# Kernel tuning notes

Hardware: AMD Instinct MI355X
Metric: run time of the kernel (lower is better)

## Reference

```python
import jax, jax.numpy as jnp
import numpy as np

R = 8          # num_real
P = 8          # num_complex_conjugate_pairs
L = 4          # num_layers (hidden Linear+ReLU blocks)
H = 256        # hidden_dim
B = 16384      # batch


def _init_params(key, C, out_dim):
    ks = jax.random.split(key, 6)
    s_in = 1.0  # fan_in = 1
    s_h = 1.0 / np.sqrt(H)
    return dict(
        W_in=jax.random.uniform(ks[0], (C, H), jnp.float32, -s_in, s_in),
        b_in=jax.random.uniform(ks[1], (C, H), jnp.float32, -s_in, s_in),
        W_h=jax.random.uniform(ks[2], (L, C, H, H), jnp.float32, -s_h, s_h),
        b_h=jax.random.uniform(ks[3], (L, C, H), jnp.float32, -s_h, s_h),
        W_out=jax.random.uniform(ks[4], (C, out_dim, H), jnp.float32, -s_h, s_h),
        b_out=jax.random.uniform(ks[5], (C, out_dim), jnp.float32, -s_h, s_h),
    )


def setup_inputs() -> dict:
    key = jax.random.key(0)
    kz, kr, kc = jax.random.split(key, 3)
    z = jax.random.normal(kz, (B, R + 2 * P), jnp.float32)
    pr = _init_params(kr, R, 1)   # real-eigenvalue MLPs, out_dim=1
    pc = _init_params(kc, P, 2)   # complex-pair MLPs, out_dim=2
    return {
        "z": z,
        "Wr_in": pr["W_in"], "br_in": pr["b_in"],
        "Wr_h": pr["W_h"], "br_h": pr["b_h"],
        "Wr_out": pr["W_out"], "br_out": pr["b_out"],
        "Wc_in": pc["W_in"], "bc_in": pc["b_in"],
        "Wc_h": pc["W_h"], "bc_h": pc["b_h"],
        "Wc_out": pc["W_out"], "bc_out": pc["b_out"],
    }


def _grouped_mlp(x, W_in, b_in, W_h, b_h, W_out, b_out):
    # x: [B, C] scalar input per channel; all C tiny MLPs run as grouped GEMMs.
    h = jax.nn.relu(x[..., None] * W_in + b_in)            # [B, C, H]
    for l in range(W_h.shape[0]):
        h = jax.nn.relu(jnp.einsum('bci,coi->bco', h, W_h[l]) + b_h[l])
    return jnp.einsum('bci,coi->bco', h, W_out) + b_out     # [B, C, out]


def reference(z, Wr_in, br_in, Wr_h, br_h, Wr_out, br_out,
              Wc_in, bc_in, Wc_h, bc_h, Wc_out, bc_out):
    # real channels: z[..., i] -> Linear chains -> real_lambda [B, R]
    real_lambda = _grouped_mlp(z[..., :R], Wr_in, br_in, Wr_h, br_h,
                               Wr_out, br_out)[..., 0]
    # complex pairs: magnitude z_r^2 + z_i^2 per pair -> (mu, omega)
    z_mag = z[..., R::2] ** 2 + z[..., R + 1::2] ** 2        # [B, P]
    mu_omega = _grouped_mlp(z_mag, Wc_in, bc_in, Wc_h, bc_h,
                            Wc_out, bc_out)                  # [B, P, 2]
    mu = mu_omega[..., 0]
    omega = mu_omega[..., 1]
    return real_lambda, mu, omega
```

## Files before the change

### kernel.cpp

```cpp
#include <hip/hip_runtime.h>

#define OUT_MU 131072
#define OUT_OM 262144
#define BIAS_OFF 4194304
#define WOUT_OFF 4210688

typedef _Float16 half8 __attribute__((ext_vector_type(8)));
typedef _Float16 half4 __attribute__((ext_vector_type(4)));
typedef float    floatx16 __attribute__((ext_vector_type(16)));

__device__ __forceinline__ void wait_lgkm0() {
    asm volatile("s_waitcnt lgkmcnt(0)" ::: "memory");
}
__device__ __forceinline__ void wait_vm0() {
    asm volatile("s_waitcnt vmcnt(0)" ::: "memory");
}
__device__ __forceinline__ void barrier_raw() {
    asm volatile("s_barrier" ::: "memory");
}

#define AS1 __attribute__((address_space(1)))
#define AS3 __attribute__((address_space(3)))

__global__ void prep_w(const float* __restrict__ Wr_h,
                       const float* __restrict__ Wc_h,
                       _Float16* __restrict__ dst) {
    int v = blockIdx.x * 256 + threadIdx.x;
    int lane = v & 63;
    int nt   = (v >> 6) & 1;
    int wv   = (v >> 7) & 3;
    int ks   = (v >> 9) & 15;
    int l    = (v >> 13) & 3;
    int ch   = v >> 15;
    int n  = wv * 64 + nt * 32 + (lane & 31);
    int k0 = ks * 16 + (lane >> 5) * 8;
    const float* src = (ch < 8) ? Wr_h : Wc_h;
    int c = ch & 7;
    const float* p = src + ((size_t)((l * 8 + c) * 256 + n)) * 256 + k0;
    float4 a = *(const float4*)p;
    float4 b = *(const float4*)(p + 4);
    half8 o;
    o[0] = (_Float16)a.x; o[1] = (_Float16)a.y; o[2] = (_Float16)a.z; o[3] = (_Float16)a.w;
    o[4] = (_Float16)b.x; o[5] = (_Float16)b.y; o[6] = (_Float16)b.z; o[7] = (_Float16)b.w;
    *(half8*)(dst + (size_t)v * 8) = o;
}

__global__ void prep_b(const float* __restrict__ br_h,
                       const float* __restrict__ bc_h,
                       _Float16* __restrict__ dst) {
    int t = blockIdx.x * 256 + threadIdx.x;
    int e  = t & 3;
    int q  = (t >> 2) & 3;
    int nt = (t >> 4) & 1;
    int hi = (t >> 5) & 1;
    int wv = (t >> 6) & 3;
    int l  = (t >> 8) & 3;
    int ch = (t >> 10) & 15;
    int n = wv * 64 + nt * 32 + q * 8 + hi * 4 + e;
    const float* src = (ch < 8) ? br_h : bc_h;
    dst[BIAS_OFF + t] = (_Float16)src[(l * 8 + (ch & 7)) * 256 + n];
}

__global__ void prep_wo(const float* __restrict__ Wr_out,
                        const float* __restrict__ Wc_out,
                        _Float16* __restrict__ dst) {
    int t = blockIdx.x * 256 + threadIdx.x;
    int j = t & 255, d = (t >> 8) & 1, ch = t >> 9;
    int c = ch & 7;
    float v;
    if (ch < 8) v = d ? 0.f : Wr_out[c * 256 + j];
    else        v = Wc_out[(c * 2 + d) * 256 + j];
    dst[WOUT_OFF + t] = (_Float16)v;
}

__global__ __launch_bounds__(256, 2)
void mlp_fused(const float* __restrict__ z,
               const float* __restrict__ Wr_in, const float* __restrict__ br_in,
               const float* __restrict__ Wc_in, const float* __restrict__ bc_in,
               const float* __restrict__ br_out, const float* __restrict__ bc_out,
               const _Float16* __restrict__ wst,
               float* __restrict__ out) {
    __shared__ __align__(16) char smem[77824];
    const int tid  = threadIdx.x;
    const int lane = tid & 63;
    const int wv   = tid >> 6;
    const int bid  = blockIdx.x;
    const int ch   = bid & 15;
    const int m0   = (bid >> 4) * 128;
    const bool isC = ch >= 8;
    const int c    = ch & 7;
    const int hi   = lane >> 5;
    const int r32  = lane & 31;
    float* zbuf = (float*)(smem + 65536);

    {
        const float* zs = z + (size_t)m0 * 24 + wv * 768 + lane * 4;
        char* zd = smem + 65536 + wv * 3072;
        __builtin_amdgcn_global_load_lds((const AS1 void*)zs,         (AS3 void*)zd,          16, 0, 0);
        __builtin_amdgcn_global_load_lds((const AS1 void*)(zs + 256), (AS3 void*)(zd + 1024), 16, 0, 0);
        __builtin_amdgcn_global_load_lds((const AS1 void*)(zs + 512), (AS3 void*)(zd + 2048), 16, 0, 0);
    }

    const half8* wl = (const half8*)wst + (size_t)ch * 32768 + wv * 128 + lane;

    half8 wr[2][2];
    #pragma unroll
    for (int nt = 0; nt < 2; ++nt) wr[0][nt] = wl[nt * 64];

    int vb[4];
    #pragma unroll
    for (int mt = 0; mt < 4; ++mt)
        vb[mt] = (mt * 32 + r32) * 512 + ((hi ^ (lane & 7)) << 4);

    const int jg = tid & 31;
    const int rg = tid >> 5;
    const float* Wi = (isC ? Wc_in : Wr_in) + c * 256 + jg * 8;
    const float* bi = (isC ? bc_in : br_in) + c * 256 + jg * 8;
    float4 w0 = *(const float4*)Wi;
    float4 w1 = *(const float4*)(Wi + 4);
    float4 v0 = *(const float4*)bi;
    float4 v1 = *(const float4*)(bi + 4);

    wait_vm0();

    {
        #pragma unroll
        for (int i = 0; i < 16; ++i) {
            int m = rg * 16 + i;
            float x;
            if (!isC) x = zbuf[m * 24 + c];
            else {
                float2 p = *(const float2*)(zbuf + m * 24 + 8 + 2 * c);
                x = p.x * p.x + p.y * p.y;
            }
            half8 o;
            o[0] = (_Float16)fmaxf(fmaf(x, w0.x, v0.x), 0.f);
            o[1] = (_Float16)fmaxf(fmaf(x, w0.y, v0.y), 0.f);
            o[2] = (_Float16)fmaxf(fmaf(x, w0.z, v0.z), 0.f);
            o[3] = (_Float16)fmaxf(fmaf(x, w0.w, v0.w), 0.f);
            o[4] = (_Float16)fmaxf(fmaf(x, w1.x, v1.x), 0.f);
            o[5] = (_Float16)fmaxf(fmaf(x, w1.y, v1.y), 0.f);
            o[6] = (_Float16)fmaxf(fmaf(x, w1.z, v1.z), 0.f);
            o[7] = (_Float16)fmaxf(fmaf(x, w1.w, v1.w), 0.f);
            *(half8*)(smem + m * 512 + ((jg ^ (m & 7)) << 4)) = o;
        }
    }
    wait_lgkm0();
    barrier_raw();

    const half8* bpc = (const half8*)(wst + BIAS_OFF) + ((ch * 4) * 4 + wv) * 8 + hi * 4;

    #pragma unroll 1
    for (int l = 0; l < 4; ++l) {
        const half8* bl = bpc + l * 32;
        half8 bb0 = bl[0], bb1 = bl[1], bb2 = bl[2], bb3 = bl[3];

        floatx16 acc[2][4];
        #pragma unroll
        for (int a = 0; a < 2; ++a)
            #pragma unroll
            for (int b = 0; b < 4; ++b) acc[a][b] = 0.f;

        half8 bfr[2][4];
        #pragma unroll
        for (int mt = 0; mt < 4; ++mt)
            bfr[0][mt] = *(const half8*)(smem + vb[mt]);

        #pragma unroll
        for (int ks = 0; ks < 16; ++ks) {
            {
                const half8* p = wl + (ks + 1) * 512;
                wr[(ks + 1) & 1][0] = p[0];
                wr[(ks + 1) & 1][1] = p[64];
            }
            if (ks < 15) {
                #pragma unroll
                for (int mt = 0; mt < 4; ++mt)
                    bfr[(ks + 1) & 1][mt] =
                        *(const half8*)(smem + (vb[mt] ^ ((ks + 1) << 5)));
            }
            __builtin_amdgcn_s_setprio(1);
            #pragma unroll
            for (int nt = 0; nt < 2; ++nt)
                #pragma unroll
                for (int mt = 0; mt < 4; ++mt)
                    acc[nt][mt] = __builtin_amdgcn_mfma_f32_32x32x16_f16(
                        wr[ks & 1][nt], bfr[ks & 1][mt], acc[nt][mt], 0, 0, 0);
            __builtin_amdgcn_s_setprio(0);
        }
        wl += 8192;

        wait_lgkm0();
        barrier_raw();
        #pragma unroll
        for (int nt = 0; nt < 2; ++nt) {
            #pragma unroll
            for (int q = 0; q < 4; ++q) {
                half8 bv = (nt * 2 + (q >> 1)) == 0 ? bb0 :
                           (nt * 2 + (q >> 1)) == 1 ? bb1 :
                           (nt * 2 + (q >> 1)) == 2 ? bb2 : bb3;
                const int be = (q & 1) * 4;
                float b0 = (float)bv[be + 0];
                float b1 = (float)bv[be + 1];
                float b2 = (float)bv[be + 2];
                float b3 = (float)bv[be + 3];
                const int slot = wv * 8 + nt * 4 + q;
                #pragma unroll
                for (int mt = 0; mt < 4; ++mt) {
                    const int m = mt * 32 + r32;
                    half4 o;
                    o[0] = (_Float16)fmaxf(acc[nt][mt][4 * q + 0] + b0, 0.f);
                    o[1] = (_Float16)fmaxf(acc[nt][mt][4 * q + 1] + b1, 0.f);
                    o[2] = (_Float16)fmaxf(acc[nt][mt][4 * q + 2] + b2, 0.f);
                    o[3] = (_Float16)fmaxf(acc[nt][mt][4 * q + 3] + b3, 0.f);
                    *(half4*)(smem + m * 512 + ((slot ^ (m & 7)) << 4) + hi * 8) = o;
                }
            }
        }
        wait_lgkm0();
        barrier_raw();
    }

    {
        const int q = tid & 1, m = tid >> 1;
        const half8* Wo = (const half8*)(wst + WOUT_OFF) + ch * 64 + q * 16;
        float s0 = 0.f, s1 = 0.f;
        #pragma unroll
        for (int i = 0; i < 16; ++i) {
            int slot = q * 16 + i;
            half8 hv = *(const half8*)(smem + m * 512 + ((slot ^ (m & 7)) << 4));
            half8 wo0 = Wo[i];
            #pragma unroll
            for (int e = 0; e < 8; ++e) s0 = fmaf((float)hv[e], (float)wo0[e], s0);
            if (isC) {
                half8 wo1 = Wo[32 + i];
                #pragma unroll
                for (int e = 0; e < 8; ++e) s1 = fmaf((float)hv[e], (float)wo1[e], s1);
            }
        }
        s0 += __shfl_xor(s0, 1);
        if (isC) s1 += __shfl_xor(s1, 1);
        if (q == 0) {
            const int row = m0 + m;
            if (!isC) {
                out[row * 8 + c] = s0 + br_out[c];
            } else {
                out[OUT_MU + row * 8 + c] = s0 + bc_out[c * 2];
                out[OUT_OM + row * 8 + c] = s1 + bc_out[c * 2 + 1];
            }
        }
    }
}

extern "C" void kernel_launch(void* const* d_in, const int* in_sizes, int n_in,
                              void* d_out, int out_size, void* d_ws, size_t ws_size,
                              hipStream_t stream) {
    const float* z      = (const float*)d_in[0];
    const float* Wr_in  = (const float*)d_in[1];
    const float* br_in  = (const float*)d_in[2];
    const float* Wr_h   = (const float*)d_in[3];
    const float* br_h   = (const float*)d_in[4];
    const float* Wr_out = (const float*)d_in[5];
    const float* br_out = (const float*)d_in[6];
    const float* Wc_in  = (const float*)d_in[7];
    const float* bc_in  = (const float*)d_in[8];
    const float* Wc_h   = (const float*)d_in[9];
    const float* bc_h   = (const float*)d_in[10];
    const float* Wc_out = (const float*)d_in[11];
    const float* bc_out = (const float*)d_in[12];
    _Float16* wst = (_Float16*)d_ws;
    float* out = (float*)d_out;

    prep_w<<<2048, 256, 0, stream>>>(Wr_h, Wc_h, wst);
    prep_b<<<64, 256, 0, stream>>>(br_h, bc_h, wst);
    prep_wo<<<32, 256, 0, stream>>>(Wr_out, Wc_out, wst);
    mlp_fused<<<2048, 256, 0, stream>>>(z, Wr_in, br_in, Wc_in, bc_in,
                                        br_out, bc_out, wst, out);
}
```

Measured before the change: 146.3 us.

## Split each 128-row tile across eight waves with deeper weight prefetch

The fused MLP block grows from 4 to 8 waves. Each wave now computes a 64x64 output tile: waves are split by column group and by row half, so MFMA accumulators per wave drop from 8 to 4. Weight fragments are prefetched two k-steps ahead in a 4-deep register ring, and the output dot product and input layer are spread over more threads. The aim is more latency hiding and higher occupancy, at the cost of each weight fragment being loaded by two waves instead of one. An extra barrier is added after the z load.

```diff
diff --git a/kernel.cpp b/kernel.cpp
--- a/kernel.cpp
+++ b/kernel.cpp
@@ -73,7 +73,7 @@
     dst[WOUT_OFF + t] = (_Float16)v;
 }
 
-__global__ __launch_bounds__(256, 2)
+__global__ __launch_bounds__(512, 4)
 void mlp_fused(const float* __restrict__ z,
                const float* __restrict__ Wr_in, const float* __restrict__ br_in,
                const float* __restrict__ Wc_in, const float* __restrict__ bc_in,
@@ -84,6 +84,8 @@
     const int tid  = threadIdx.x;
     const int lane = tid & 63;
     const int wv   = tid >> 6;
+    const int wr   = wv & 3;
+    const int wc   = wv >> 2;
     const int bid  = blockIdx.x;
     const int ch   = bid & 15;
     const int m0   = (bid >> 4) * 128;
@@ -93,7 +95,7 @@
     const int r32  = lane & 31;
     float* zbuf = (float*)(smem + 65536);
 
-    {
+    if (wv < 4) {
         const float* zs = z + (size_t)m0 * 24 + wv * 768 + lane * 4;
         char* zd = smem + 65536 + wv * 3072;
         __builtin_amdgcn_global_load_lds((const AS1 void*)zs,         (AS3 void*)zd,          16, 0, 0);
@@ -101,16 +103,13 @@
         __builtin_amdgcn_global_load_lds((const AS1 void*)(zs + 512), (AS3 void*)(zd + 2048), 16, 0, 0);
     }
 
-    const half8* wl = (const half8*)wst + (size_t)ch * 32768 + wv * 128 + lane;
-
-    half8 wr[2][2];
-    #pragma unroll
-    for (int nt = 0; nt < 2; ++nt) wr[0][nt] = wl[nt * 64];
-
-    int vb[4];
-    #pragma unroll
-    for (int mt = 0; mt < 4; ++mt)
-        vb[mt] = (mt * 32 + r32) * 512 + ((hi ^ (lane & 7)) << 4);
+    const half8* wl = (const half8*)wst + (size_t)ch * 32768 + wr * 128 + lane;
+
+    half8 wreg[4][2];
+    wreg[0][0] = wl[0];   wreg[0][1] = wl[64];
+    wreg[1][0] = wl[512]; wreg[1][1] = wl[576];
+
+    const int vb = (wc * 64 + r32) * 512 + ((hi ^ (lane & 7)) << 4);
 
     const int jg = tid & 31;
     const int rg = tid >> 5;
@@ -122,11 +121,12 @@
     float4 v1 = *(const float4*)(bi + 4);
 
     wait_vm0();
+    barrier_raw();
 
     {
         #pragma unroll
-        for (int i = 0; i < 16; ++i) {
-            int m = rg * 16 + i;
+        for (int i = 0; i < 8; ++i) {
+            int m = rg * 8 + i;
             float x;
             if (!isC) x = zbuf[m * 24 + c];
             else {
@@ -148,47 +148,47 @@
     wait_lgkm0();
     barrier_raw();
 
-    const half8* bpc = (const half8*)(wst + BIAS_OFF) + ((ch * 4) * 4 + wv) * 8 + hi * 4;
+    const half8* bpc = (const half8*)(wst + BIAS_OFF) + ((ch * 4) * 4 + wr) * 8 + hi * 4;
 
     #pragma unroll 1
     for (int l = 0; l < 4; ++l) {
+        floatx16 acc[2][2];
+        #pragma unroll
+        for (int a = 0; a < 2; ++a)
+            #pragma unroll
+            for (int b = 0; b < 2; ++b) acc[a][b] = 0.f;
+
+        half8 bfr[2][2];
+        bfr[0][0] = *(const half8*)(smem + vb);
+        bfr[0][1] = *(const half8*)(smem + vb + 16384);
+
+        #pragma unroll
+        for (int ks = 0; ks < 16; ++ks) {
+            {
+                const half8* p = wl + (ks + 2) * 512;
+                wreg[(ks + 2) & 3][0] = p[0];
+                wreg[(ks + 2) & 3][1] = p[64];
+            }
+            if (ks < 15) {
+                const int na = vb ^ ((ks + 1) << 5);
+                bfr[(ks + 1) & 1][0] = *(const half8*)(smem + na);
+                bfr[(ks + 1) & 1][1] = *(const half8*)(smem + na + 16384);
+            }
+            __builtin_amdgcn_s_setprio(1);
+            acc[0][0] = __builtin_amdgcn_mfma_f32_32x32x16_f16(
+                wreg[ks & 3][0], bfr[ks & 1][0], acc[0][0], 0, 0, 0);
+            acc[0][1] = __builtin_amdgcn_mfma_f32_32x32x16_f16(
+                wreg[ks & 3][0], bfr[ks & 1][1], acc[0][1], 0, 0, 0);
+            acc[1][0] = __builtin_amdgcn_mfma_f32_32x32x16_f16(
+                wreg[ks & 3][1], bfr[ks & 1][0], acc[1][0], 0, 0, 0);
+            acc[1][1] = __builtin_amdgcn_mfma_f32_32x32x16_f16(
+                wreg[ks & 3][1], bfr[ks & 1][1], acc[1][1], 0, 0, 0);
+            __builtin_amdgcn_s_setprio(0);
+        }
+        wl += 8192;
+
         const half8* bl = bpc + l * 32;
         half8 bb0 = bl[0], bb1 = bl[1], bb2 = bl[2], bb3 = bl[3];
-
-        floatx16 acc[2][4];
-        #pragma unroll
-        for (int a = 0; a < 2; ++a)
-            #pragma unroll
-            for (int b = 0; b < 4; ++b) acc[a][b] = 0.f;
-
-        half8 bfr[2][4];
-        #pragma unroll
-        for (int mt = 0; mt < 4; ++mt)
-            bfr[0][mt] = *(const half8*)(smem + vb[mt]);
-
-        #pragma unroll
-        for (int ks = 0; ks < 16; ++ks) {
-            {
-                const half8* p = wl + (ks + 1) * 512;
-                wr[(ks + 1) & 1][0] = p[0];
-                wr[(ks + 1) & 1][1] = p[64];
-            }
-            if (ks < 15) {
-                #pragma unroll
-                for (int mt = 0; mt < 4; ++mt)
-                    bfr[(ks + 1) & 1][mt] =
-                        *(const half8*)(smem + (vb[mt] ^ ((ks + 1) << 5)));
-            }
-            __builtin_amdgcn_s_setprio(1);
-            #pragma unroll
-            for (int nt = 0; nt < 2; ++nt)
-                #pragma unroll
-                for (int mt = 0; mt < 4; ++mt)
-                    acc[nt][mt] = __builtin_amdgcn_mfma_f32_32x32x16_f16(
-                        wr[ks & 1][nt], bfr[ks & 1][mt], acc[nt][mt], 0, 0, 0);
-            __builtin_amdgcn_s_setprio(0);
-        }
-        wl += 8192;
 
         wait_lgkm0();
         barrier_raw();
@@ -204,10 +204,10 @@
                 float b1 = (float)bv[be + 1];
                 float b2 = (float)bv[be + 2];
                 float b3 = (float)bv[be + 3];
-                const int slot = wv * 8 + nt * 4 + q;
+                const int slot = wr * 8 + nt * 4 + q;
                 #pragma unroll
-                for (int mt = 0; mt < 4; ++mt) {
-                    const int m = mt * 32 + r32;
+                for (int mt = 0; mt < 2; ++mt) {
+                    const int m = wc * 64 + mt * 32 + r32;
                     half4 o;
                     o[0] = (_Float16)fmaxf(acc[nt][mt][4 * q + 0] + b0, 0.f);
                     o[1] = (_Float16)fmaxf(acc[nt][mt][4 * q + 1] + b1, 0.f);
@@ -222,24 +222,24 @@
     }
 
     {
-        const int q = tid & 1, m = tid >> 1;
-        const half8* Wo = (const half8*)(wst + WOUT_OFF) + ch * 64 + q * 16;
+        const int q = tid & 3, m = tid >> 2;
+        const half8* Wo = (const half8*)(wst + WOUT_OFF) + ch * 64;
         float s0 = 0.f, s1 = 0.f;
         #pragma unroll
-        for (int i = 0; i < 16; ++i) {
-            int slot = q * 16 + i;
+        for (int i = 0; i < 8; ++i) {
+            int slot = q * 8 + i;
             half8 hv = *(const half8*)(smem + m * 512 + ((slot ^ (m & 7)) << 4));
-            half8 wo0 = Wo[i];
+            half8 wo0 = Wo[slot];
             #pragma unroll
             for (int e = 0; e < 8; ++e) s0 = fmaf((float)hv[e], (float)wo0[e], s0);
             if (isC) {
-                half8 wo1 = Wo[32 + i];
+                half8 wo1 = Wo[32 + slot];
                 #pragma unroll
                 for (int e = 0; e < 8; ++e) s1 = fmaf((float)hv[e], (float)wo1[e], s1);
             }
         }
-        s0 += __shfl_xor(s0, 1);
-        if (isC) s1 += __shfl_xor(s1, 1);
+        s0 += __shfl_xor(s0, 1); s0 += __shfl_xor(s0, 2);
+        if (isC) { s1 += __shfl_xor(s1, 1); s1 += __shfl_xor(s1, 2); }
         if (q == 0) {
             const int row = m0 + m;
             if (!isC) {
@@ -274,6 +274,6 @@
     prep_w<<<2048, 256, 0, stream>>>(Wr_h, Wc_h, wst);
     prep_b<<<64, 256, 0, stream>>>(br_h, bc_h, wst);
     prep_wo<<<32, 256, 0, stream>>>(Wr_out, Wc_out, wst);
-    mlp_fused<<<2048, 256, 0, stream>>>(z, Wr_in, br_in, Wc_in, bc_in,
+    mlp_fused<<<2048, 512, 0, stream>>>(z, Wr_in, br_in, Wc_in, bc_in,
                                         br_out, bc_out, wst, out);
 }
```

Result: slower. 173.9 us (+18.9%).

## Retile MLP GEMM warps into a 2x2 grid of 128 N by 64 M

Applied to the files above, without the earlier changes.

Each of the four waves now covers a 128-column by 64-row output tile (four N-tiles by two M-tiles) instead of 64 columns by all 128 rows. The weight and bias prepack layouts are reindexed to match. Per K-step each wave loads four weight fragments from global memory and two activation fragments from LDS, where before it loaded two and four. The intent is to cut LDS read traffic and bank pressure, at the cost of doubling per-wave global weight loads and their register footprint. An extra barrier is added after the z load, and the bias loads move to after the K loop.

```diff
diff --git a/kernel.cpp b/kernel.cpp
--- a/kernel.cpp
+++ b/kernel.cpp
@@ -27,13 +27,13 @@
                        _Float16* __restrict__ dst) {
     int v = blockIdx.x * 256 + threadIdx.x;
     int lane = v & 63;
-    int nt   = (v >> 6) & 1;
-    int wv   = (v >> 7) & 3;
-    int ks   = (v >> 9) & 15;
+    int nt   = (v >> 6) & 3;
+    int wr   = (v >> 8) & 1;
+    int kst  = (v >> 9) & 15;
     int l    = (v >> 13) & 3;
     int ch   = v >> 15;
-    int n  = wv * 64 + nt * 32 + (lane & 31);
-    int k0 = ks * 16 + (lane >> 5) * 8;
+    int n  = wr * 128 + nt * 32 + (lane & 31);
+    int k0 = kst * 16 + (lane >> 5) * 8;
     const float* src = (ch < 8) ? Wr_h : Wc_h;
     int c = ch & 7;
     const float* p = src + ((size_t)((l * 8 + c) * 256 + n)) * 256 + k0;
@@ -51,12 +51,12 @@
     int t = blockIdx.x * 256 + threadIdx.x;
     int e  = t & 3;
     int q  = (t >> 2) & 3;
-    int nt = (t >> 4) & 1;
-    int hi = (t >> 5) & 1;
-    int wv = (t >> 6) & 3;
+    int nt = (t >> 4) & 3;
+    int hi = (t >> 6) & 1;
+    int wr = (t >> 7) & 1;
     int l  = (t >> 8) & 3;
     int ch = (t >> 10) & 15;
-    int n = wv * 64 + nt * 32 + q * 8 + hi * 4 + e;
+    int n = wr * 128 + nt * 32 + q * 8 + hi * 4 + e;
     const float* src = (ch < 8) ? br_h : bc_h;
     dst[BIAS_OFF + t] = (_Float16)src[(l * 8 + (ch & 7)) * 256 + n];
 }
@@ -84,6 +84,8 @@
     const int tid  = threadIdx.x;
     const int lane = tid & 63;
     const int wv   = tid >> 6;
+    const int wr   = wv & 1;
+    const int wc   = wv >> 1;
     const int bid  = blockIdx.x;
     const int ch   = bid & 15;
     const int m0   = (bid >> 4) * 128;
@@ -101,16 +103,13 @@
         __builtin_amdgcn_global_load_lds((const AS1 void*)(zs + 512), (AS3 void*)(zd + 2048), 16, 0, 0);
     }
 
-    const half8* wl = (const half8*)wst + (size_t)ch * 32768 + wv * 128 + lane;
-
-    half8 wr[2][2];
+    const half8* wl = (const half8*)wst + (size_t)ch * 32768 + wr * 256 + lane;
+
+    half8 wreg[2][4];
     #pragma unroll
-    for (int nt = 0; nt < 2; ++nt) wr[0][nt] = wl[nt * 64];
-
-    int vb[4];
-    #pragma unroll
-    for (int mt = 0; mt < 4; ++mt)
-        vb[mt] = (mt * 32 + r32) * 512 + ((hi ^ (lane & 7)) << 4);
+    for (int nt = 0; nt < 4; ++nt) wreg[0][nt] = wl[nt * 64];
+
+    const int vbase = (wc * 64 + r32) * 512 + (((r32 & 7) ^ hi) << 4);
 
     const int jg = tid & 31;
     const int rg = tid >> 5;
@@ -122,6 +121,7 @@
     float4 v1 = *(const float4*)(bi + 4);
 
     wait_vm0();
+    barrier_raw();
 
     {
         #pragma unroll
@@ -148,66 +148,67 @@
     wait_lgkm0();
     barrier_raw();
 
-    const half8* bpc = (const half8*)(wst + BIAS_OFF) + ((ch * 4) * 4 + wv) * 8 + hi * 4;
+    const half8* bbase = (const half8*)(wst + BIAS_OFF);
 
     #pragma unroll 1
     for (int l = 0; l < 4; ++l) {
-        const half8* bl = bpc + l * 32;
-        half8 bb0 = bl[0], bb1 = bl[1], bb2 = bl[2], bb3 = bl[3];
-
-        floatx16 acc[2][4];
-        #pragma unroll
-        for (int a = 0; a < 2; ++a)
-            #pragma unroll
-            for (int b = 0; b < 4; ++b) acc[a][b] = 0.f;
-
-        half8 bfr[2][4];
-        #pragma unroll
-        for (int mt = 0; mt < 4; ++mt)
-            bfr[0][mt] = *(const half8*)(smem + vb[mt]);
+        floatx16 acc[4][2];
+        #pragma unroll
+        for (int a = 0; a < 4; ++a)
+            #pragma unroll
+            for (int b = 0; b < 2; ++b) acc[a][b] = 0.f;
+
+        half8 bfr[2][2];
+        bfr[0][0] = *(const half8*)(smem + vbase);
+        bfr[0][1] = *(const half8*)(smem + vbase + 16384);
 
         #pragma unroll
         for (int ks = 0; ks < 16; ++ks) {
             {
                 const half8* p = wl + (ks + 1) * 512;
-                wr[(ks + 1) & 1][0] = p[0];
-                wr[(ks + 1) & 1][1] = p[64];
+                #pragma unroll
+                for (int nt = 0; nt < 4; ++nt) wreg[(ks + 1) & 1][nt] = p[nt * 64];
             }
             if (ks < 15) {
-                #pragma unroll
-                for (int mt = 0; mt < 4; ++mt)
-                    bfr[(ks + 1) & 1][mt] =
-                        *(const half8*)(smem + (vb[mt] ^ ((ks + 1) << 5)));
+                const int na = vbase ^ ((ks + 1) << 5);
+                bfr[(ks + 1) & 1][0] = *(const half8*)(smem + na);
+                bfr[(ks + 1) & 1][1] = *(const half8*)(smem + na + 16384);
             }
             __builtin_amdgcn_s_setprio(1);
             #pragma unroll
-            for (int nt = 0; nt < 2; ++nt)
-                #pragma unroll
-                for (int mt = 0; mt < 4; ++mt)
+            for (int nt = 0; nt < 4; ++nt)
+                #pragma unroll
+                for (int mt = 0; mt < 2; ++mt)
                     acc[nt][mt] = __builtin_amdgcn_mfma_f32_32x32x16_f16(
-                        wr[ks & 1][nt], bfr[ks & 1][mt], acc[nt][mt], 0, 0, 0);
+                        wreg[ks & 1][nt], bfr[ks & 1][mt], acc[nt][mt], 0, 0, 0);
             __builtin_amdgcn_s_setprio(0);
         }
         wl += 8192;
+
+        half8 bq[8];
+        {
+            const half8* bl = bbase + ((((ch * 4 + l) * 2 + wr) * 2 + hi) * 8);
+            #pragma unroll
+            for (int j = 0; j < 8; ++j) bq[j] = bl[j];
+        }
 
         wait_lgkm0();
         barrier_raw();
         #pragma unroll
-        for (int nt = 0; nt < 2; ++nt) {
+        for (int nt = 0; nt < 4; ++nt) {
             #pragma unroll
             for (int q = 0; q < 4; ++q) {
-                half8 bv = (nt * 2 + (q >> 1)) == 0 ? bb0 :
-                           (nt * 2 + (q >> 1)) == 1 ? bb1 :
-                           (nt * 2 + (q >> 1)) == 2 ? bb2 : bb3;
+                half8 bv = bq[nt * 2 + (q >> 1)];
                 const int be = (q & 1) * 4;
                 float b0 = (float)bv[be + 0];
                 float b1 = (float)bv[be + 1];
                 float b2 = (float)bv[be + 2];
                 float b3 = (float)bv[be + 3];
-                const int slot = wv * 8 + nt * 4 + q;
-                #pragma unroll
-                for (int mt = 0; mt < 4; ++mt) {
-                    const int m = mt * 32 + r32;
+                const int nb = wr * 128 + nt * 32 + q * 8 + hi * 4;
+                const int slot = nb >> 3;
+                #pragma unroll
+                for (int mt = 0; mt < 2; ++mt) {
+                    const int m = wc * 64 + mt * 32 + r32;
                     half4 o;
                     o[0] = (_Float16)fmaxf(acc[nt][mt][4 * q + 0] + b0, 0.f);
                     o[1] = (_Float16)fmaxf(acc[nt][mt][4 * q + 1] + b1, 0.f);
```

Result: slower. 153.6 us (+5.0%).
